# Kernel optimization log

Measured on AMD Instinct MI355X. Metric: run time of the kernel, lower is better.

The kernel has to match this reference:

```python
import jax, jax.numpy as jnp
import numpy as np

B, STATE, OBS = 131072, 16, 8


def _spd(key, b, n, scale=0.1):
    a = jax.random.normal(key, (b, n, n), dtype=jnp.float32) * scale
    return a @ jnp.swapaxes(a, -1, -2) + jnp.eye(n, dtype=jnp.float32)


def setup_inputs() -> dict:
    key = jax.random.key(0)
    ks = jax.random.split(key, 7)
    return {
        "input": jax.random.normal(ks[0], (B, OBS), dtype=jnp.float32),
        "mean": jax.random.normal(ks[1], (B, STATE), dtype=jnp.float32),
        "cov": _spd(ks[2], B, STATE),
        "H": jax.random.normal(ks[3], (B, OBS, STATE), dtype=jnp.float32) * 0.3,
        "R": _spd(ks[4], B, OBS),
        "F": jax.random.normal(ks[5], (B, STATE, STATE), dtype=jnp.float32) * 0.1,
        "Q": _spd(ks[6], B, STATE),
    }


def reference(input, mean, cov, H, R, F, Q):
    # ---- update (no NaNs in input, so the full-batch path is taken) ----
    Ht = jnp.swapaxes(H, -1, -2)                      # [B, s, o]
    S = H @ cov @ Ht + R                              # system covariance [B, o, o]
    PHt = cov @ Ht                                    # [B, s, o]
    # torch.solve(B, A) solves A X = B with A = S^T, B = (cov H^T)^T; K = X^T
    Kt = jnp.linalg.solve(jnp.swapaxes(S, -1, -2), jnp.swapaxes(PHt, -1, -2))
    K = jnp.swapaxes(Kt, -1, -2)                      # Kalman gain [B, s, o]
    resid = input - jnp.einsum('bos,bs->bo', H, mean)  # innovation [B, o]
    new_mean = mean + jnp.einsum('bso,bo->bs', K, resid)
    # Joseph-stabilized covariance update
    I = jnp.eye(cov.shape[-1], dtype=cov.dtype)
    p1 = I - K @ H                                    # [B, s, s]
    new_cov = p1 @ cov @ jnp.swapaxes(p1, -1, -2) + K @ R @ jnp.swapaxes(K, -1, -2)
    # ---- predict ----
    pred_mean = jnp.einsum('bij,bj->bi', F, new_mean)
    pred_cov = F @ new_cov @ jnp.swapaxes(F, -1, -2) + Q
    return pred_mean, pred_cov
```

## Files before the change

### kernel.cpp

```cpp
#include <hip/hip_runtime.h>
#include <math.h>


#define NB 131072
#define NSTATE 16
#define NOBS 8
#define BATCH_PER_BLOCK 8
#define THREADS (BATCH_PER_BLOCK * 16)

#define LDS_PER 1000

__global__ void __launch_bounds__(THREADS)
kalman_step_kernel(const float* __restrict__ input, const float* __restrict__ mean,
                   const float* __restrict__ cov, const float* __restrict__ H,
                   const float* __restrict__ R, const float* __restrict__ F,
                   const float* __restrict__ Q,
                   float* __restrict__ out_mean, float* __restrict__ out_cov)
{
    __shared__ __align__(16) float lds[BATCH_PER_BLOCK * LDS_PER];

    const int tid = threadIdx.x;
    const int g = tid >> 4;
    const int t = tid & 15;
    const long b = (long)blockIdx.x * BATCH_PER_BLOCK + g;

    float* Lb    = lds + g * LDS_PER;
    float* covA  = Lb;
    float* Hb    = Lb + 256;
    float* Rb    = Lb + 392;
    float* PHtb  = Lb + 464;
    float* Sb    = Lb + 608;
    float* p1T   = Lb + 680;
    float* meanv = Lb + 936;
    float* nmeanv= Lb + 952;
    float* residv= Lb + 968;

    float freg[16];
    {
        const float4* F4 = (const float4*)(F + b * 256 + t * 16);
        float4 f0 = F4[0], f1 = F4[1], f2 = F4[2], f3 = F4[3];
        freg[0]=f0.x; freg[1]=f0.y; freg[2]=f0.z; freg[3]=f0.w;
        freg[4]=f1.x; freg[5]=f1.y; freg[6]=f1.z; freg[7]=f1.w;
        freg[8]=f2.x; freg[9]=f2.y; freg[10]=f2.z; freg[11]=f2.w;
        freg[12]=f3.x; freg[13]=f3.y; freg[14]=f3.z; freg[15]=f3.w;
    }
    float covrow[16];
    {
        const float4* C4 = (const float4*)(cov + b * 256 + t * 16);
        float4 c0 = C4[0], c1 = C4[1], c2 = C4[2], c3 = C4[3];
        covrow[0]=c0.x; covrow[1]=c0.y; covrow[2]=c0.z; covrow[3]=c0.w;
        covrow[4]=c1.x; covrow[5]=c1.y; covrow[6]=c1.z; covrow[7]=c1.w;
        covrow[8]=c2.x; covrow[9]=c2.y; covrow[10]=c2.z; covrow[11]=c2.w;
        covrow[12]=c3.x; covrow[13]=c3.y; covrow[14]=c3.z; covrow[15]=c3.w;
        float4* cd = (float4*)(covA + t * 16);
        cd[0]=c0; cd[1]=c1; cd[2]=c2; cd[3]=c3;
    }
    const float m = mean[b * 16 + t];
    meanv[t] = m;
    float inp = 0.0f;
    if (t < NOBS) {
        inp = input[b * 8 + t];
        const float4* H4 = (const float4*)(H + b * 128 + t * 16);
        float4 h0 = H4[0], h1 = H4[1], h2 = H4[2], h3 = H4[3];
        float* hd = Hb + t * 17;
        hd[0]=h0.x; hd[1]=h0.y; hd[2]=h0.z; hd[3]=h0.w;
        hd[4]=h1.x; hd[5]=h1.y; hd[6]=h1.z; hd[7]=h1.w;
        hd[8]=h2.x; hd[9]=h2.y; hd[10]=h2.z; hd[11]=h2.w;
        hd[12]=h3.x; hd[13]=h3.y; hd[14]=h3.z; hd[15]=h3.w;
        const float4* R4 = (const float4*)(R + b * 64 + t * 8);
        float4 r0 = R4[0], r1 = R4[1];
        float* rd = Rb + t * 9;
        rd[0]=r0.x; rd[1]=r0.y; rd[2]=r0.z; rd[3]=r0.w;
        rd[4]=r1.x; rd[5]=r1.y; rd[6]=r1.z; rd[7]=r1.w;
    }
    __syncthreads();

    float pht[8];
    #pragma unroll
    for (int o = 0; o < 8; ++o) {
        float acc = 0.0f;
        #pragma unroll
        for (int j = 0; j < 16; ++j) acc += covrow[j] * Hb[o * 17 + j];
        pht[o] = acc;
        PHtb[t * 9 + o] = acc;
    }
    if (t < NOBS) {
        float acc = inp;
        #pragma unroll
        for (int s = 0; s < 16; ++s) acc -= Hb[t * 17 + s] * meanv[s];
        residv[t] = acc;
    }
    __syncthreads();

    if (t < NOBS) {
        float sreg[8];
        #pragma unroll
        for (int c = 0; c < 8; ++c) sreg[c] = Rb[t * 9 + c];
        #pragma unroll
        for (int s = 0; s < 16; ++s) {
            float h = Hb[t * 17 + s];
            #pragma unroll
            for (int c = 0; c < 8; ++c) sreg[c] += h * PHtb[s * 9 + c];
        }
        #pragma unroll
        for (int c = 0; c < 8; ++c) Sb[t * 9 + c] = sreg[c];
    }
    __syncthreads();

    float Lm[8][8];
    #pragma unroll
    for (int i = 0; i < 8; ++i)
        #pragma unroll
        for (int j = 0; j <= i; ++j)
            Lm[i][j] = Sb[i * 9 + j];
    float dinv[8];
    #pragma unroll
    for (int k = 0; k < 8; ++k) {
        float diag = Lm[k][k];
        #pragma unroll
        for (int j = 0; j < k; ++j) diag -= Lm[k][j] * Lm[k][j];
        float lkk = sqrtf(diag);
        float inv = 1.0f / lkk;
        dinv[k] = inv;
        #pragma unroll
        for (int i = k + 1; i < 8; ++i) {
            float v = Lm[i][k];
            #pragma unroll
            for (int j = 0; j < k; ++j) v -= Lm[i][j] * Lm[k][j];
            Lm[i][k] = v * inv;
        }
    }
    float yv[8];
    #pragma unroll
    for (int i = 0; i < 8; ++i) {
        float v = pht[i];
        #pragma unroll
        for (int j = 0; j < i; ++j) v -= Lm[i][j] * yv[j];
        yv[i] = v * dinv[i];
    }
    float Kr[8];
    #pragma unroll
    for (int i = 7; i >= 0; --i) {
        float v = yv[i];
        #pragma unroll
        for (int j = i + 1; j < 8; ++j) v -= Lm[j][i] * Kr[j];
        Kr[i] = v * dinv[i];
    }
    {
        float nm = m;
        #pragma unroll
        for (int o = 0; o < 8; ++o) nm += Kr[o] * residv[o];
        nmeanv[t] = nm;
    }
    #pragma unroll
    for (int o = 0; o < 8; ++o) PHtb[o * 16 + t] = Kr[o];
    __syncthreads();

    float p1[16];
    #pragma unroll
    for (int j = 0; j < 16; ++j) p1[j] = (j == t) ? 1.0f : 0.0f;
    #pragma unroll
    for (int o = 0; o < 8; ++o) {
        float ko = Kr[o];
        #pragma unroll
        for (int j = 0; j < 16; ++j) p1[j] -= ko * Hb[o * 17 + j];
    }
    #pragma unroll
    for (int j = 0; j < 16; ++j) p1T[j * 16 + t] = p1[j];
    float KRr[8];
    #pragma unroll
    for (int c = 0; c < 8; ++c) KRr[c] = 0.0f;
    #pragma unroll
    for (int o = 0; o < 8; ++o) {
        float ko = Kr[o];
        #pragma unroll
        for (int c = 0; c < 8; ++c) KRr[c] += ko * Rb[o * 9 + c];
    }
    __syncthreads();

    float tmp[16];
    #pragma unroll
    for (int k = 0; k < 16; ++k) tmp[k] = 0.0f;
    #pragma unroll
    for (int j = 0; j < 16; ++j) {
        float pj = p1[j];
        const float4* cr = (const float4*)(covA + j * 16);
        float4 c0 = cr[0], c1 = cr[1], c2 = cr[2], c3 = cr[3];
        tmp[0]+=pj*c0.x; tmp[1]+=pj*c0.y; tmp[2]+=pj*c0.z; tmp[3]+=pj*c0.w;
        tmp[4]+=pj*c1.x; tmp[5]+=pj*c1.y; tmp[6]+=pj*c1.z; tmp[7]+=pj*c1.w;
        tmp[8]+=pj*c2.x; tmp[9]+=pj*c2.y; tmp[10]+=pj*c2.z; tmp[11]+=pj*c2.w;
        tmp[12]+=pj*c3.x; tmp[13]+=pj*c3.y; tmp[14]+=pj*c3.z; tmp[15]+=pj*c3.w;
    }

    float nc[16];
    #pragma unroll
    for (int j = 0; j < 16; ++j) nc[j] = 0.0f;
    #pragma unroll
    for (int k = 0; k < 16; ++k) {
        float tk = tmp[k];
        const float4* pr = (const float4*)(p1T + k * 16);
        float4 c0 = pr[0], c1 = pr[1], c2 = pr[2], c3 = pr[3];
        nc[0]+=tk*c0.x; nc[1]+=tk*c0.y; nc[2]+=tk*c0.z; nc[3]+=tk*c0.w;
        nc[4]+=tk*c1.x; nc[5]+=tk*c1.y; nc[6]+=tk*c1.z; nc[7]+=tk*c1.w;
        nc[8]+=tk*c2.x; nc[9]+=tk*c2.y; nc[10]+=tk*c2.z; nc[11]+=tk*c2.w;
        nc[12]+=tk*c3.x; nc[13]+=tk*c3.y; nc[14]+=tk*c3.z; nc[15]+=tk*c3.w;
    }
    #pragma unroll
    for (int o = 0; o < 8; ++o) {
        float ko = KRr[o];
        const float4* kr = (const float4*)(PHtb + o * 16);
        float4 c0 = kr[0], c1 = kr[1], c2 = kr[2], c3 = kr[3];
        nc[0]+=ko*c0.x; nc[1]+=ko*c0.y; nc[2]+=ko*c0.z; nc[3]+=ko*c0.w;
        nc[4]+=ko*c1.x; nc[5]+=ko*c1.y; nc[6]+=ko*c1.z; nc[7]+=ko*c1.w;
        nc[8]+=ko*c2.x; nc[9]+=ko*c2.y; nc[10]+=ko*c2.z; nc[11]+=ko*c2.w;
        nc[12]+=ko*c3.x; nc[13]+=ko*c3.y; nc[14]+=ko*c3.z; nc[15]+=ko*c3.w;
    }
    __syncthreads();

    {
        float4* cd = (float4*)(covA + t * 16);
        cd[0] = make_float4(nc[0], nc[1], nc[2], nc[3]);
        cd[1] = make_float4(nc[4], nc[5], nc[6], nc[7]);
        cd[2] = make_float4(nc[8], nc[9], nc[10], nc[11]);
        cd[3] = make_float4(nc[12], nc[13], nc[14], nc[15]);
    }
    #pragma unroll
    for (int j = 0; j < 16; ++j) p1T[j * 16 + t] = freg[j];
    __syncthreads();

    const float4* Q4 = (const float4*)(Q + b * 256 + t * 16);
    float4 q0 = Q4[0], q1 = Q4[1], q2 = Q4[2], q3 = Q4[3];

    float fp[16];
    #pragma unroll
    for (int k = 0; k < 16; ++k) fp[k] = 0.0f;
    #pragma unroll
    for (int j = 0; j < 16; ++j) {
        float fj = freg[j];
        const float4* cr = (const float4*)(covA + j * 16);
        float4 c0 = cr[0], c1 = cr[1], c2 = cr[2], c3 = cr[3];
        fp[0]+=fj*c0.x; fp[1]+=fj*c0.y; fp[2]+=fj*c0.z; fp[3]+=fj*c0.w;
        fp[4]+=fj*c1.x; fp[5]+=fj*c1.y; fp[6]+=fj*c1.z; fp[7]+=fj*c1.w;
        fp[8]+=fj*c2.x; fp[9]+=fj*c2.y; fp[10]+=fj*c2.z; fp[11]+=fj*c2.w;
        fp[12]+=fj*c3.x; fp[13]+=fj*c3.y; fp[14]+=fj*c3.z; fp[15]+=fj*c3.w;
    }
    float pm = 0.0f;
    #pragma unroll
    for (int j = 0; j < 16; ++j) pm += freg[j] * nmeanv[j];

    float pc[16];
    pc[0]=q0.x; pc[1]=q0.y; pc[2]=q0.z; pc[3]=q0.w;
    pc[4]=q1.x; pc[5]=q1.y; pc[6]=q1.z; pc[7]=q1.w;
    pc[8]=q2.x; pc[9]=q2.y; pc[10]=q2.z; pc[11]=q2.w;
    pc[12]=q3.x; pc[13]=q3.y; pc[14]=q3.z; pc[15]=q3.w;
    #pragma unroll
    for (int k = 0; k < 16; ++k) {
        float fk = fp[k];
        const float4* fr = (const float4*)(p1T + k * 16);
        float4 c0 = fr[0], c1 = fr[1], c2 = fr[2], c3 = fr[3];
        pc[0]+=fk*c0.x; pc[1]+=fk*c0.y; pc[2]+=fk*c0.z; pc[3]+=fk*c0.w;
        pc[4]+=fk*c1.x; pc[5]+=fk*c1.y; pc[6]+=fk*c1.z; pc[7]+=fk*c1.w;
        pc[8]+=fk*c2.x; pc[9]+=fk*c2.y; pc[10]+=fk*c2.z; pc[11]+=fk*c2.w;
        pc[12]+=fk*c3.x; pc[13]+=fk*c3.y; pc[14]+=fk*c3.z; pc[15]+=fk*c3.w;
    }

    out_mean[b * 16 + t] = pm;
    {
        float4* od = (float4*)(out_cov + b * 256 + t * 16);
        od[0] = make_float4(pc[0], pc[1], pc[2], pc[3]);
        od[1] = make_float4(pc[4], pc[5], pc[6], pc[7]);
        od[2] = make_float4(pc[8], pc[9], pc[10], pc[11]);
        od[3] = make_float4(pc[12], pc[13], pc[14], pc[15]);
    }
}

extern "C" void kernel_launch(void* const* d_in, const int* in_sizes, int n_in,
                              void* d_out, int out_size, void* d_ws, size_t ws_size,
                              hipStream_t stream) {
    const float* input = (const float*)d_in[0];
    const float* mean  = (const float*)d_in[1];
    const float* cov   = (const float*)d_in[2];
    const float* H     = (const float*)d_in[3];
    const float* R     = (const float*)d_in[4];
    const float* F     = (const float*)d_in[5];
    const float* Q     = (const float*)d_in[6];
    float* out = (float*)d_out;
    float* out_mean = out;
    float* out_cov  = out + (size_t)NB * NSTATE;

    dim3 grid(NB / BATCH_PER_BLOCK);
    dim3 block(THREADS);
    hipLaunchKernelGGL(kalman_step_kernel, grid, block, 0, stream,
                       input, mean, cov, H, R, F, Q, out_mean, out_cov);
}
```

Before: 524.2 us.

## Shrink LDS per batch, use single-wave blocks, keep H/R in registers

Blocks shrink to one 64-thread wave handling 4 batch items, and the per-item LDS scratch shrinks from 1000 to 616 floats. This is done by reusing one matrix buffer for cov, the intermediate products and F, removing the padded H/R layouts in favour of float4-aligned rows, and keeping H and R rows in registers. The F and Q loads are deferred until they are needed, and the matrix products are restructured so that both operands of each step are read as transposed rows from LDS. The aim is higher occupancy and vectorized LDS traffic, at the cost of a few extra barriers and more LDS write-backs of intermediates.

```diff
diff --git a/kernel.cpp b/kernel.cpp
--- a/kernel.cpp
+++ b/kernel.cpp
@@ -3,47 +3,48 @@
 
 
 #define NB 131072
-#define NSTATE 16
-#define NOBS 8
-#define BATCH_PER_BLOCK 8
-#define THREADS (BATCH_PER_BLOCK * 16)
-
-#define LDS_PER 1000
-
-__global__ void __launch_bounds__(THREADS)
+#define BPB 4
+#define THREADS 64
+#define LDS_PER 616
+
+#define ROW_FMA16(acc, s, base) do {                                        \
+    const float4* _r = (const float4*)(base);                               \
+    float4 _c0=_r[0], _c1=_r[1], _c2=_r[2], _c3=_r[3];                      \
+    acc[0]+=(s)*_c0.x; acc[1]+=(s)*_c0.y; acc[2]+=(s)*_c0.z; acc[3]+=(s)*_c0.w; \
+    acc[4]+=(s)*_c1.x; acc[5]+=(s)*_c1.y; acc[6]+=(s)*_c1.z; acc[7]+=(s)*_c1.w; \
+    acc[8]+=(s)*_c2.x; acc[9]+=(s)*_c2.y; acc[10]+=(s)*_c2.z; acc[11]+=(s)*_c2.w; \
+    acc[12]+=(s)*_c3.x; acc[13]+=(s)*_c3.y; acc[14]+=(s)*_c3.z; acc[15]+=(s)*_c3.w; \
+} while (0)
+
+#define ROW_FMA8(acc, s, base) do {                                         \
+    const float4* _r = (const float4*)(base);                               \
+    float4 _c0=_r[0], _c1=_r[1];                                            \
+    acc[0]+=(s)*_c0.x; acc[1]+=(s)*_c0.y; acc[2]+=(s)*_c0.z; acc[3]+=(s)*_c0.w; \
+    acc[4]+=(s)*_c1.x; acc[5]+=(s)*_c1.y; acc[6]+=(s)*_c1.z; acc[7]+=(s)*_c1.w; \
+} while (0)
+
+__global__ void __launch_bounds__(THREADS, 4)
 kalman_step_kernel(const float* __restrict__ input, const float* __restrict__ mean,
                    const float* __restrict__ cov, const float* __restrict__ H,
                    const float* __restrict__ R, const float* __restrict__ F,
                    const float* __restrict__ Q,
                    float* __restrict__ out_mean, float* __restrict__ out_cov)
 {
-    __shared__ __align__(16) float lds[BATCH_PER_BLOCK * LDS_PER];
+    __shared__ __align__(16) float lds[BPB * LDS_PER];
 
     const int tid = threadIdx.x;
     const int g = tid >> 4;
     const int t = tid & 15;
-    const long b = (long)blockIdx.x * BATCH_PER_BLOCK + g;
+    const long b = (long)blockIdx.x * BPB + g;
 
     float* Lb    = lds + g * LDS_PER;
-    float* covA  = Lb;
+    float* Mb    = Lb;
     float* Hb    = Lb + 256;
-    float* Rb    = Lb + 392;
-    float* PHtb  = Lb + 464;
-    float* Sb    = Lb + 608;
-    float* p1T   = Lb + 680;
-    float* meanv = Lb + 936;
-    float* nmeanv= Lb + 952;
-    float* residv= Lb + 968;
-
-    float freg[16];
-    {
-        const float4* F4 = (const float4*)(F + b * 256 + t * 16);
-        float4 f0 = F4[0], f1 = F4[1], f2 = F4[2], f3 = F4[3];
-        freg[0]=f0.x; freg[1]=f0.y; freg[2]=f0.z; freg[3]=f0.w;
-        freg[4]=f1.x; freg[5]=f1.y; freg[6]=f1.z; freg[7]=f1.w;
-        freg[8]=f2.x; freg[9]=f2.y; freg[10]=f2.z; freg[11]=f2.w;
-        freg[12]=f3.x; freg[13]=f3.y; freg[14]=f3.z; freg[15]=f3.w;
-    }
+    float* Rb    = Lb + 384;
+    float* Xb    = Lb + 448;
+    float* meanv = Lb + 576;
+    float* rn    = Lb + 592;
+
     float covrow[16];
     {
         const float4* C4 = (const float4*)(cov + b * 256 + t * 16);
@@ -52,67 +53,86 @@
         covrow[4]=c1.x; covrow[5]=c1.y; covrow[6]=c1.z; covrow[7]=c1.w;
         covrow[8]=c2.x; covrow[9]=c2.y; covrow[10]=c2.z; covrow[11]=c2.w;
         covrow[12]=c3.x; covrow[13]=c3.y; covrow[14]=c3.z; covrow[15]=c3.w;
-        float4* cd = (float4*)(covA + t * 16);
-        cd[0]=c0; cd[1]=c1; cd[2]=c2; cd[3]=c3;
+        float4* md = (float4*)(Mb + t * 16);
+        md[0]=c0; md[1]=c1; md[2]=c2; md[3]=c3;
     }
     const float m = mean[b * 16 + t];
     meanv[t] = m;
+
+    float hreg[16];
+    float rreg[8];
     float inp = 0.0f;
-    if (t < NOBS) {
+    if (t < 8) {
         inp = input[b * 8 + t];
         const float4* H4 = (const float4*)(H + b * 128 + t * 16);
         float4 h0 = H4[0], h1 = H4[1], h2 = H4[2], h3 = H4[3];
-        float* hd = Hb + t * 17;
-        hd[0]=h0.x; hd[1]=h0.y; hd[2]=h0.z; hd[3]=h0.w;
-        hd[4]=h1.x; hd[5]=h1.y; hd[6]=h1.z; hd[7]=h1.w;
-        hd[8]=h2.x; hd[9]=h2.y; hd[10]=h2.z; hd[11]=h2.w;
-        hd[12]=h3.x; hd[13]=h3.y; hd[14]=h3.z; hd[15]=h3.w;
+        hreg[0]=h0.x; hreg[1]=h0.y; hreg[2]=h0.z; hreg[3]=h0.w;
+        hreg[4]=h1.x; hreg[5]=h1.y; hreg[6]=h1.z; hreg[7]=h1.w;
+        hreg[8]=h2.x; hreg[9]=h2.y; hreg[10]=h2.z; hreg[11]=h2.w;
+        hreg[12]=h3.x; hreg[13]=h3.y; hreg[14]=h3.z; hreg[15]=h3.w;
+        float4* hd = (float4*)(Hb + t * 16);
+        hd[0]=h0; hd[1]=h1; hd[2]=h2; hd[3]=h3;
         const float4* R4 = (const float4*)(R + b * 64 + t * 8);
         float4 r0 = R4[0], r1 = R4[1];
-        float* rd = Rb + t * 9;
-        rd[0]=r0.x; rd[1]=r0.y; rd[2]=r0.z; rd[3]=r0.w;
-        rd[4]=r1.x; rd[5]=r1.y; rd[6]=r1.z; rd[7]=r1.w;
+        rreg[0]=r0.x; rreg[1]=r0.y; rreg[2]=r0.z; rreg[3]=r0.w;
+        rreg[4]=r1.x; rreg[5]=r1.y; rreg[6]=r1.z; rreg[7]=r1.w;
+        float4* rd = (float4*)(Rb + t * 8);
+        rd[0]=r0; rd[1]=r1;
     }
     __syncthreads();
 
     float pht[8];
     #pragma unroll
     for (int o = 0; o < 8; ++o) {
-        float acc = 0.0f;
-        #pragma unroll
-        for (int j = 0; j < 16; ++j) acc += covrow[j] * Hb[o * 17 + j];
+        const float4* hr = (const float4*)(Hb + o * 16);
+        float4 h0 = hr[0], h1 = hr[1], h2 = hr[2], h3 = hr[3];
+        float acc;
+        acc  = covrow[0]*h0.x + covrow[1]*h0.y + covrow[2]*h0.z + covrow[3]*h0.w;
+        acc += covrow[4]*h1.x + covrow[5]*h1.y + covrow[6]*h1.z + covrow[7]*h1.w;
+        acc += covrow[8]*h2.x + covrow[9]*h2.y + covrow[10]*h2.z + covrow[11]*h2.w;
+        acc += covrow[12]*h3.x + covrow[13]*h3.y + covrow[14]*h3.z + covrow[15]*h3.w;
         pht[o] = acc;
-        PHtb[t * 9 + o] = acc;
-    }
-    if (t < NOBS) {
+    }
+    {
+        float4* pd = (float4*)(Xb + t * 8);
+        pd[0] = make_float4(pht[0], pht[1], pht[2], pht[3]);
+        pd[1] = make_float4(pht[4], pht[5], pht[6], pht[7]);
+    }
+    if (t < 8) {
+        const float4* mv = (const float4*)meanv;
+        float4 m0 = mv[0], m1 = mv[1], m2 = mv[2], m3 = mv[3];
         float acc = inp;
-        #pragma unroll
-        for (int s = 0; s < 16; ++s) acc -= Hb[t * 17 + s] * meanv[s];
-        residv[t] = acc;
-    }
-    __syncthreads();
-
-    if (t < NOBS) {
+        acc -= hreg[0]*m0.x + hreg[1]*m0.y + hreg[2]*m0.z + hreg[3]*m0.w;
+        acc -= hreg[4]*m1.x + hreg[5]*m1.y + hreg[6]*m1.z + hreg[7]*m1.w;
+        acc -= hreg[8]*m2.x + hreg[9]*m2.y + hreg[10]*m2.z + hreg[11]*m2.w;
+        acc -= hreg[12]*m3.x + hreg[13]*m3.y + hreg[14]*m3.z + hreg[15]*m3.w;
+        rn[t] = acc;
+    }
+    __syncthreads();
+
+    if (t < 8) {
         float sreg[8];
         #pragma unroll
-        for (int c = 0; c < 8; ++c) sreg[c] = Rb[t * 9 + c];
+        for (int c = 0; c < 8; ++c) sreg[c] = rreg[c];
         #pragma unroll
         for (int s = 0; s < 16; ++s) {
-            float h = Hb[t * 17 + s];
-            #pragma unroll
-            for (int c = 0; c < 8; ++c) sreg[c] += h * PHtb[s * 9 + c];
+            float h = hreg[s];
+            ROW_FMA8(sreg, h, Xb + s * 8);
         }
-        #pragma unroll
-        for (int c = 0; c < 8; ++c) Sb[t * 9 + c] = sreg[c];
+        float4* sd = (float4*)(Xb + t * 8);
+        sd[0] = make_float4(sreg[0], sreg[1], sreg[2], sreg[3]);
+        sd[1] = make_float4(sreg[4], sreg[5], sreg[6], sreg[7]);
     }
     __syncthreads();
 
     float Lm[8][8];
     #pragma unroll
-    for (int i = 0; i < 8; ++i)
-        #pragma unroll
-        for (int j = 0; j <= i; ++j)
-            Lm[i][j] = Sb[i * 9 + j];
+    for (int i = 0; i < 8; ++i) {
+        const float4* sr = (const float4*)(Xb + i * 8);
+        float4 s0 = sr[0], s1 = sr[1];
+        Lm[i][0]=s0.x; Lm[i][1]=s0.y; Lm[i][2]=s0.z; Lm[i][3]=s0.w;
+        Lm[i][4]=s1.x; Lm[i][5]=s1.y; Lm[i][6]=s1.z; Lm[i][7]=s1.w;
+    }
     float dinv[8];
     #pragma unroll
     for (int k = 0; k < 8; ++k) {
@@ -147,89 +167,81 @@
         Kr[i] = v * dinv[i];
     }
     {
+        const float4* rv = (const float4*)rn;
+        float4 r0 = rv[0], r1 = rv[1];
         float nm = m;
-        #pragma unroll
-        for (int o = 0; o < 8; ++o) nm += Kr[o] * residv[o];
-        nmeanv[t] = nm;
-    }
-    #pragma unroll
-    for (int o = 0; o < 8; ++o) PHtb[o * 16 + t] = Kr[o];
-    __syncthreads();
-
-    float p1[16];
-    #pragma unroll
-    for (int j = 0; j < 16; ++j) p1[j] = (j == t) ? 1.0f : 0.0f;
+        nm += Kr[0]*r0.x + Kr[1]*r0.y + Kr[2]*r0.z + Kr[3]*r0.w;
+        nm += Kr[4]*r1.x + Kr[5]*r1.y + Kr[6]*r1.z + Kr[7]*r1.w;
+        rn[t] = nm;
+    }
+    #pragma unroll
+    for (int o = 0; o < 8; ++o) Xb[o * 16 + t] = Kr[o];
+    __syncthreads();
+
+    const float4* F4 = (const float4*)(F + b * 256 + t * 16);
+    float4 fA = F4[0], fB = F4[1], fC = F4[2], fD = F4[3];
+
+    float p1r[16];
+    #pragma unroll
+    for (int j = 0; j < 16; ++j) p1r[j] = (j == t) ? 1.0f : 0.0f;
+    #pragma unroll
+    for (int o = 0; o < 8; ++o) {
+        float nko = -Kr[o];
+        ROW_FMA16(p1r, nko, Hb + o * 16);
+    }
+    float KRr[8];
+    #pragma unroll
+    for (int c = 0; c < 8; ++c) KRr[c] = 0.0f;
     #pragma unroll
     for (int o = 0; o < 8; ++o) {
         float ko = Kr[o];
-        #pragma unroll
-        for (int j = 0; j < 16; ++j) p1[j] -= ko * Hb[o * 17 + j];
-    }
-    #pragma unroll
-    for (int j = 0; j < 16; ++j) p1T[j * 16 + t] = p1[j];
-    float KRr[8];
-    #pragma unroll
-    for (int c = 0; c < 8; ++c) KRr[c] = 0.0f;
-    #pragma unroll
-    for (int o = 0; o < 8; ++o) {
-        float ko = Kr[o];
-        #pragma unroll
-        for (int c = 0; c < 8; ++c) KRr[c] += ko * Rb[o * 9 + c];
-    }
-    __syncthreads();
+        ROW_FMA8(KRr, ko, Rb + o * 8);
+    }
 
     float tmp[16];
     #pragma unroll
     for (int k = 0; k < 16; ++k) tmp[k] = 0.0f;
     #pragma unroll
     for (int j = 0; j < 16; ++j) {
-        float pj = p1[j];
-        const float4* cr = (const float4*)(covA + j * 16);
-        float4 c0 = cr[0], c1 = cr[1], c2 = cr[2], c3 = cr[3];
-        tmp[0]+=pj*c0.x; tmp[1]+=pj*c0.y; tmp[2]+=pj*c0.z; tmp[3]+=pj*c0.w;
-        tmp[4]+=pj*c1.x; tmp[5]+=pj*c1.y; tmp[6]+=pj*c1.z; tmp[7]+=pj*c1.w;
-        tmp[8]+=pj*c2.x; tmp[9]+=pj*c2.y; tmp[10]+=pj*c2.z; tmp[11]+=pj*c2.w;
-        tmp[12]+=pj*c3.x; tmp[13]+=pj*c3.y; tmp[14]+=pj*c3.z; tmp[15]+=pj*c3.w;
-    }
+        float pj = p1r[j];
+        ROW_FMA16(tmp, pj, Mb + j * 16);
+    }
+    __syncthreads();
+    #pragma unroll
+    for (int k = 0; k < 16; ++k) Mb[k * 16 + t] = tmp[k];
+    __syncthreads();
+
+    const float4* Q4 = (const float4*)(Q + b * 256 + t * 16);
+    float4 qA = Q4[0], qB = Q4[1], qC = Q4[2], qD = Q4[3];
 
     float nc[16];
     #pragma unroll
     for (int j = 0; j < 16; ++j) nc[j] = 0.0f;
     #pragma unroll
     for (int k = 0; k < 16; ++k) {
-        float tk = tmp[k];
-        const float4* pr = (const float4*)(p1T + k * 16);
-        float4 c0 = pr[0], c1 = pr[1], c2 = pr[2], c3 = pr[3];
-        nc[0]+=tk*c0.x; nc[1]+=tk*c0.y; nc[2]+=tk*c0.z; nc[3]+=tk*c0.w;
-        nc[4]+=tk*c1.x; nc[5]+=tk*c1.y; nc[6]+=tk*c1.z; nc[7]+=tk*c1.w;
-        nc[8]+=tk*c2.x; nc[9]+=tk*c2.y; nc[10]+=tk*c2.z; nc[11]+=tk*c2.w;
-        nc[12]+=tk*c3.x; nc[13]+=tk*c3.y; nc[14]+=tk*c3.z; nc[15]+=tk*c3.w;
+        float pk = p1r[k];
+        ROW_FMA16(nc, pk, Mb + k * 16);
     }
     #pragma unroll
     for (int o = 0; o < 8; ++o) {
         float ko = KRr[o];
-        const float4* kr = (const float4*)(PHtb + o * 16);
-        float4 c0 = kr[0], c1 = kr[1], c2 = kr[2], c3 = kr[3];
-        nc[0]+=ko*c0.x; nc[1]+=ko*c0.y; nc[2]+=ko*c0.z; nc[3]+=ko*c0.w;
-        nc[4]+=ko*c1.x; nc[5]+=ko*c1.y; nc[6]+=ko*c1.z; nc[7]+=ko*c1.w;
-        nc[8]+=ko*c2.x; nc[9]+=ko*c2.y; nc[10]+=ko*c2.z; nc[11]+=ko*c2.w;
-        nc[12]+=ko*c3.x; nc[13]+=ko*c3.y; nc[14]+=ko*c3.z; nc[15]+=ko*c3.w;
-    }
-    __syncthreads();
-
-    {
-        float4* cd = (float4*)(covA + t * 16);
-        cd[0] = make_float4(nc[0], nc[1], nc[2], nc[3]);
-        cd[1] = make_float4(nc[4], nc[5], nc[6], nc[7]);
-        cd[2] = make_float4(nc[8], nc[9], nc[10], nc[11]);
-        cd[3] = make_float4(nc[12], nc[13], nc[14], nc[15]);
-    }
-    #pragma unroll
-    for (int j = 0; j < 16; ++j) p1T[j * 16 + t] = freg[j];
-    __syncthreads();
-
-    const float4* Q4 = (const float4*)(Q + b * 256 + t * 16);
-    float4 q0 = Q4[0], q1 = Q4[1], q2 = Q4[2], q3 = Q4[3];
+        ROW_FMA16(nc, ko, Xb + o * 16);
+    }
+    __syncthreads();
+    {
+        float4* md = (float4*)(Mb + t * 16);
+        md[0] = make_float4(nc[0], nc[1], nc[2], nc[3]);
+        md[1] = make_float4(nc[4], nc[5], nc[6], nc[7]);
+        md[2] = make_float4(nc[8], nc[9], nc[10], nc[11]);
+        md[3] = make_float4(nc[12], nc[13], nc[14], nc[15]);
+    }
+    __syncthreads();
+
+    float freg[16];
+    freg[0]=fA.x; freg[1]=fA.y; freg[2]=fA.z; freg[3]=fA.w;
+    freg[4]=fB.x; freg[5]=fB.y; freg[6]=fB.z; freg[7]=fB.w;
+    freg[8]=fC.x; freg[9]=fC.y; freg[10]=fC.z; freg[11]=fC.w;
+    freg[12]=fD.x; freg[13]=fD.y; freg[14]=fD.z; freg[15]=fD.w;
 
     float fp[16];
     #pragma unroll
@@ -237,31 +249,31 @@
     #pragma unroll
     for (int j = 0; j < 16; ++j) {
         float fj = freg[j];
-        const float4* cr = (const float4*)(covA + j * 16);
-        float4 c0 = cr[0], c1 = cr[1], c2 = cr[2], c3 = cr[3];
-        fp[0]+=fj*c0.x; fp[1]+=fj*c0.y; fp[2]+=fj*c0.z; fp[3]+=fj*c0.w;
-        fp[4]+=fj*c1.x; fp[5]+=fj*c1.y; fp[6]+=fj*c1.z; fp[7]+=fj*c1.w;
-        fp[8]+=fj*c2.x; fp[9]+=fj*c2.y; fp[10]+=fj*c2.z; fp[11]+=fj*c2.w;
-        fp[12]+=fj*c3.x; fp[13]+=fj*c3.y; fp[14]+=fj*c3.z; fp[15]+=fj*c3.w;
-    }
-    float pm = 0.0f;
-    #pragma unroll
-    for (int j = 0; j < 16; ++j) pm += freg[j] * nmeanv[j];
+        ROW_FMA16(fp, fj, Mb + j * 16);
+    }
+    float pm;
+    {
+        const float4* rv = (const float4*)rn;
+        float4 r0 = rv[0], r1 = rv[1], r2 = rv[2], r3 = rv[3];
+        pm  = freg[0]*r0.x + freg[1]*r0.y + freg[2]*r0.z + freg[3]*r0.w;
+        pm += freg[4]*r1.x + freg[5]*r1.y + freg[6]*r1.z + freg[7]*r1.w;
+        pm += freg[8]*r2.x + freg[9]*r2.y + freg[10]*r2.z + freg[11]*r2.w;
+        pm += freg[12]*r3.x + freg[13]*r3.y + freg[14]*r3.z + freg[15]*r3.w;
+    }
+    __syncthreads();
+    #pragma unroll
+    for (int k = 0; k < 16; ++k) Mb[k * 16 + t] = fp[k];
+    __syncthreads();
 
     float pc[16];
-    pc[0]=q0.x; pc[1]=q0.y; pc[2]=q0.z; pc[3]=q0.w;
-    pc[4]=q1.x; pc[5]=q1.y; pc[6]=q1.z; pc[7]=q1.w;
-    pc[8]=q2.x; pc[9]=q2.y; pc[10]=q2.z; pc[11]=q2.w;
-    pc[12]=q3.x; pc[13]=q3.y; pc[14]=q3.z; pc[15]=q3.w;
+    pc[0]=qA.x; pc[1]=qA.y; pc[2]=qA.z; pc[3]=qA.w;
+    pc[4]=qB.x; pc[5]=qB.y; pc[6]=qB.z; pc[7]=qB.w;
+    pc[8]=qC.x; pc[9]=qC.y; pc[10]=qC.z; pc[11]=qC.w;
+    pc[12]=qD.x; pc[13]=qD.y; pc[14]=qD.z; pc[15]=qD.w;
     #pragma unroll
     for (int k = 0; k < 16; ++k) {
-        float fk = fp[k];
-        const float4* fr = (const float4*)(p1T + k * 16);
-        float4 c0 = fr[0], c1 = fr[1], c2 = fr[2], c3 = fr[3];
-        pc[0]+=fk*c0.x; pc[1]+=fk*c0.y; pc[2]+=fk*c0.z; pc[3]+=fk*c0.w;
-        pc[4]+=fk*c1.x; pc[5]+=fk*c1.y; pc[6]+=fk*c1.z; pc[7]+=fk*c1.w;
-        pc[8]+=fk*c2.x; pc[9]+=fk*c2.y; pc[10]+=fk*c2.z; pc[11]+=fk*c2.w;
-        pc[12]+=fk*c3.x; pc[13]+=fk*c3.y; pc[14]+=fk*c3.z; pc[15]+=fk*c3.w;
+        float fk = freg[k];
+        ROW_FMA16(pc, fk, Mb + k * 16);
     }
 
     out_mean[b * 16 + t] = pm;
@@ -286,9 +298,9 @@
     const float* Q     = (const float*)d_in[6];
     float* out = (float*)d_out;
     float* out_mean = out;
-    float* out_cov  = out + (size_t)NB * NSTATE;
-
-    dim3 grid(NB / BATCH_PER_BLOCK);
+    float* out_cov  = out + (size_t)NB * 16;
+
+    dim3 grid(NB / BPB);
     dim3 block(THREADS);
     hipLaunchKernelGGL(kalman_step_kernel, grid, block, 0, stream,
                        input, mean, cov, H, R, F, Q, out_mean, out_cov);
```

Result: faster. 486.1 us (-7.3%).
